# Performance work log

Hardware: AMD Instinct MI355X
Metric: run time of the kernel (lower is better)

Reference implementation:

```python
import jax, jax.numpy as jnp
import numpy as np

N_NODES = 50000
N_EDGES = 1600000
HID = 128
REST = 96  # (hidden//4) x 1e vectors = 32*3
N_MP = 2


def _linear_init(key, fan_in, fan_out):
    return jax.random.normal(key, (fan_in, fan_out), dtype=jnp.float32) / np.sqrt(fan_in)


def setup_inputs() -> dict:
    key = jax.random.key(0)
    ks = jax.random.split(key, 16)
    h = jax.random.normal(ks[0], (N_NODES, HID + REST), dtype=jnp.float32)
    edge_index = jax.random.randint(ks[1], (2, N_EDGES), 0, N_NODES, dtype=jnp.int32)
    edge_len = jax.random.uniform(ks[2], (N_EDGES,), dtype=jnp.float32) * 5.0
    # ScalarMessagePassing MLPs: Linear(2*HID+1 -> HID), SiLU, Linear(HID -> HID), stacked per layer
    mp_w1 = jnp.stack([_linear_init(ks[3 + i], 2 * HID + 1, HID) for i in range(N_MP)])
    mp_b1 = jnp.zeros((N_MP, HID), dtype=jnp.float32)
    mp_w2 = jnp.stack([_linear_init(ks[5 + i], HID, HID) for i in range(N_MP)])
    mp_b2 = jnp.zeros((N_MP, HID), dtype=jnp.float32)
    # NodeUpdateMLP: Linear(HID -> HID), SiLU, Linear(HID -> HID)
    nu_w1 = _linear_init(ks[7], HID, HID)
    nu_b1 = jnp.zeros((HID,), dtype=jnp.float32)
    nu_w2 = _linear_init(ks[8], HID, HID)
    nu_b2 = jnp.zeros((HID,), dtype=jnp.float32)
    return dict(h=h, edge_index=edge_index, edge_len=edge_len,
                mp_w1=mp_w1, mp_b1=mp_b1, mp_w2=mp_w2, mp_b2=mp_b2,
                nu_w1=nu_w1, nu_b1=nu_b1, nu_w2=nu_w2, nu_b2=nu_b2)


def _scalar_mp(scalars, sender, receiver, edge_len, w1, b1, w2, b2):
    # gather -> MLP -> index_add scatter, residual on scalar channels
    msg_in = jnp.concatenate([scalars[sender], scalars[receiver], edge_len[:, None]], axis=-1)  # [E, 2H+1]
    msgs = jax.nn.silu(msg_in @ w1 + b1) @ w2 + b2  # [E, H]
    agg = jax.ops.segment_sum(msgs, receiver, num_segments=scalars.shape[0])  # [N, H]
    return scalars + agg


def reference(h, edge_index, edge_len, mp_w1, mp_b1, mp_w2, mp_b2, nu_w1, nu_b1, nu_w2, nu_b2):
    scalars, rest = h[..., :HID], h[..., HID:]
    sender, receiver = edge_index[0], edge_index[1]
    for i in range(N_MP):
        scalars = _scalar_mp(scalars, sender, receiver, edge_len,
                             mp_w1[i], mp_b1[i], mp_w2[i], mp_b2[i])
    # NodeUpdateMLP: scalars + MLP(scalars)
    scalars = scalars + (jax.nn.silu(scalars @ nu_w1 + nu_b1) @ nu_w2 + nu_b2)
    return jnp.concatenate([scalars, rest], axis=-1)
```

## Files before the change

### kernel.cpp

```cpp
#include <hip/hip_runtime.h>
#include <hip/hip_fp16.h>


#define NFEAT 224
#define RBITS 8
#define NB 196
#define CAP 10240

typedef _Float16 v8h __attribute__((ext_vector_type(8)));
typedef _Float16 v2h __attribute__((ext_vector_type(2)));
typedef float f32x4 __attribute__((ext_vector_type(4)));

#define MFMA16(a, b, c) __builtin_amdgcn_mfma_f32_16x16x32_f16(a, b, c, 0, 0, 0)

__device__ __forceinline__ float silu_f(float x) {
    float e = __expf(-x);
    return x * __builtin_amdgcn_rcpf(1.0f + e);
}

__global__ void k_prep(const float* __restrict__ mp_w1, const float* __restrict__ mp_w2,
                       const float* __restrict__ nu_w1, const float* __restrict__ nu_w2,
                       _Float16* __restrict__ Wp, int* __restrict__ cnt,
                       const float4* __restrict__ h4, float4* __restrict__ out4, int N) {
    if (blockIdx.x < 8) {
        const float* srcs[8] = {
            mp_w1, mp_w1 + 16384, mp_w2,
            mp_w1 + 32896, mp_w1 + 32896 + 16384, mp_w2 + 16384,
            nu_w1, nu_w2
        };
        const float* W = srcs[blockIdx.x];
        _Float16* dst = Wp + (size_t)blockIdx.x * 16384;
        for (int i = 0; i < 8; ++i) {
            int u = threadIdx.x + i * 256;
            int nt = u >> 8;
            int kt = (u >> 6) & 3;
            int lane = u & 63;
            int kb = kt * 32 + (lane >> 4) * 8;
            int n = nt * 16 + (lane & 15);
#pragma unroll
            for (int j = 0; j < 8; ++j)
                dst[(size_t)u * 8 + j] = (_Float16)W[(size_t)(kb + j) * 128 + n];
        }
    } else {
        int b = blockIdx.x - 8;
        int t = threadIdx.x;
        if (b == 0 && t < NB) cnt[t] = 0;
        if (t < 240) {
            int r = b * 10 + t / 24;
            int c = t % 24;
            if (r < N) out4[(size_t)r * 56 + 32 + c] = h4[(size_t)r * 56 + 32 + c];
        }
    }
}

__global__ void cs_bucket(const int* __restrict__ recv, const int* __restrict__ sender,
                          const float* __restrict__ elen, int* __restrict__ cnt,
                          uint2* __restrict__ bp, int E, int chunk) {
    __shared__ int lhist[256];
    __shared__ int lcur[256];
    int t = threadIdx.x;
    int start = blockIdx.x * chunk;
    int end = start + chunk; if (end > E) end = E;
    lhist[t] = 0;
    __syncthreads();
    int rv[16];
#pragma unroll
    for (int j = 0; j < 16; ++j) {
        int i = start + t + j * 256;
        rv[j] = (i < end) ? recv[i] : -1;
        if (rv[j] >= 0) atomicAdd(&lhist[rv[j] >> RBITS], 1);
    }
    __syncthreads();
    if (t < NB) {
        int c = lhist[t];
        lcur[t] = t * CAP + (c ? atomicAdd(&cnt[t], c) : 0);
    }
    __syncthreads();
#pragma unroll
    for (int j = 0; j < 16; ++j) {
        int i = start + t + j * 256;
        if (i < end) {
            int r = rv[j];
            int pos = atomicAdd(&lcur[r >> RBITS], 1);
            unsigned pay = (unsigned)sender[i] |
                           ((unsigned)__half_as_ushort(__float2half_rn(elen[i])) << 16);
            bp[pos] = make_uint2((unsigned)r, pay);
        }
    }
}

__global__ void cs_csr(const int* __restrict__ cnt, const uint2* __restrict__ bp,
                       int* __restrict__ deg, int* __restrict__ rowstart,
                       unsigned* __restrict__ epack, int N) {
    __shared__ int hist[256];
    __shared__ int sh[256];
    __shared__ int lcur[256];
    int t = threadIdx.x;
    int b = blockIdx.x;
    int r0 = b << RBITS;
    int e0 = b * CAP;
    int e1 = e0 + cnt[b];
    hist[t] = 0;
    __syncthreads();
    for (int i = e0 + t; i < e1; i += 256)
        atomicAdd(&hist[(int)(bp[i].x & 255u)], 1);
    __syncthreads();
    sh[t] = hist[t];
    __syncthreads();
    for (int off = 1; off < 256; off <<= 1) {
        int add = (t >= off) ? sh[t - off] : 0;
        __syncthreads();
        sh[t] += add;
        __syncthreads();
    }
    int excl = (t == 0) ? 0 : sh[t - 1];
    lcur[t] = e0 + excl;
    int r = r0 + t;
    if (r < N) { deg[r] = hist[t]; rowstart[r] = e0 + excl; }
    __syncthreads();
    for (int i = e0 + t; i < e1; i += 256) {
        uint2 e = bp[i];
        int pos = atomicAdd(&lcur[(int)(e.x & 255u)], 1);
        epack[pos] = e.y;
    }
}


#define MM_STAGE_A_F32(Aptr, ldA)                                           \
    _Pragma("unroll") for (int i = 0; i < 4; ++i) {                         \
        int u = threadIdx.x + i * 256;                                      \
        int r = u >> 4;                                                     \
        int g = u & 15;                                                     \
        int gr = blockIdx.x * 64 + r;                                       \
        float4 x0 = make_float4(0.f, 0.f, 0.f, 0.f);                        \
        float4 x1 = x0;                                                     \
        if (gr < M) {                                                       \
            const float* s_ = (Aptr) + (size_t)gr * (ldA) + g * 8;          \
            x0 = *(const float4*)s_;                                        \
            x1 = *(const float4*)(s_ + 4);                                  \
        }                                                                   \
        v8h hv;                                                             \
        hv[0] = (_Float16)x0.x; hv[1] = (_Float16)x0.y;                     \
        hv[2] = (_Float16)x0.z; hv[3] = (_Float16)x0.w;                     \
        hv[4] = (_Float16)x1.x; hv[5] = (_Float16)x1.y;                     \
        hv[6] = (_Float16)x1.z; hv[7] = (_Float16)x1.w;                     \
        Af[((r >> 4) * 4 + (g >> 2)) * 64 + (g & 3) * 16 + (r & 15)] = hv;  \
    }

#define MM_STAGE_A_F16(Aptr)                                                \
    _Pragma("unroll") for (int i = 0; i < 4; ++i) {                         \
        int u = threadIdx.x + i * 256;                                      \
        int r = u >> 4;                                                     \
        int g = u & 15;                                                     \
        int gr = blockIdx.x * 64 + r;                                       \
        float4 x = make_float4(0.f, 0.f, 0.f, 0.f);                         \
        if (gr < M) x = *(const float4*)((Aptr) + (size_t)gr * 128 + g * 8);\
        *(float4*)&Af[((r >> 4) * 4 + (g >> 2)) * 64 + (g & 3) * 16 + (r & 15)] = x; \
    }

#define MM_WAVE_PROLOG                                                      \
    __syncthreads();                                                        \
    const int wv = threadIdx.x >> 6;                                        \
    const int lane = threadIdx.x & 63;                                      \
    const int q_ = lane >> 4;                                               \
    const int c0_ = lane & 15;                                              \
    v8h a0 = Af[(wv * 4 + 0) * 64 + lane];                                  \
    v8h a1 = Af[(wv * 4 + 1) * 64 + lane];                                  \
    v8h a2 = Af[(wv * 4 + 2) * 64 + lane];                                  \
    v8h a3 = Af[(wv * 4 + 3) * 64 + lane];                                  \
    const int grb = blockIdx.x * 64 + wv * 16 + q_ * 4;

#define MM_RELOAD_A(SRC)                                                    \
    a0 = SRC[(wv * 4 + 0) * 64 + lane];                                     \
    a1 = SRC[(wv * 4 + 1) * 64 + lane];                                     \
    a2 = SRC[(wv * 4 + 2) * 64 + lane];                                     \
    a3 = SRC[(wv * 4 + 3) * 64 + lane];

#define MM_COMPUTE_B(WPTR, ...)                                             \
    {                                                                       \
        const v8h* Bp_ = (const v8h*)(WPTR) + lane;                         \
        _Pragma("unroll") for (int nt = 0; nt < 8; ++nt) {                  \
            v8h b0 = Bp_[nt * 256];                                         \
            v8h b1v = Bp_[nt * 256 + 64];                                   \
            v8h b2v = Bp_[nt * 256 + 128];                                  \
            v8h b3v = Bp_[nt * 256 + 192];                                  \
            f32x4 c = {0.f, 0.f, 0.f, 0.f};                                 \
            c = MFMA16(a0, b0, c);                                          \
            c = MFMA16(a1, b1v, c);                                         \
            c = MFMA16(a2, b2v, c);                                         \
            c = MFMA16(a3, b3v, c);                                         \
            const int col = nt * 16 + c0_;                                  \
            __VA_ARGS__                                                     \
        }                                                                   \
    }

#define MM_EXCHANGE_IDX                                                     \
    int kt = col >> 5;                                                      \
    int o = col & 31;                                                       \
    int qp = o >> 3;                                                        \
    int j = o & 7;                                                          \
    int base = ((wv * 4 + kt) * 64 + qp * 16 + q_ * 4) * 8 + j;

__launch_bounds__(256)
__global__ void k_mm_xsrb2(const float* __restrict__ A, int ldA,
                           const _Float16* __restrict__ Wp0, const float* __restrict__ b1,
                           _Float16* __restrict__ Xs, _Float16* __restrict__ Xrb, int M) {
    __shared__ v8h Af[1024];
    MM_STAGE_A_F32(A, ldA)
    MM_WAVE_PROLOG
    MM_COMPUTE_B(Wp0, {
        _Pragma("unroll") for (int i = 0; i < 4; ++i) {
            int gr = grb + i;
            if (gr < M) Xs[(size_t)gr * 128 + col] = (_Float16)c[i];
        }
    })
    MM_COMPUTE_B(Wp0 + 16384, {
        float bc = b1[col];
        _Pragma("unroll") for (int i = 0; i < 4; ++i) {
            int gr = grb + i;
            if (gr < M) Xrb[(size_t)gr * 128 + col] = (_Float16)(c[i] + bc);
        }
    })
}

__launch_bounds__(256)
__global__ void k_mm_accxsrb(const _Float16* __restrict__ P, const _Float16* __restrict__ Ww2,
                             const float* __restrict__ b2, const int* __restrict__ deg,
                             const float* __restrict__ Sin, int ldSin,
                             float* __restrict__ Sout,
                             const _Float16* __restrict__ Wp1, const float* __restrict__ b1,
                             _Float16* __restrict__ Xs, _Float16* __restrict__ Xrb, int M) {
    __shared__ v8h Af[1024];
    __shared__ v8h Af2[1024];
    MM_STAGE_A_F16(P)
    MM_WAVE_PROLOG
    _Float16* A2 = (_Float16*)Af2;
    MM_COMPUTE_B(Ww2, {
        float bc = b2[col];
        MM_EXCHANGE_IDX
        _Pragma("unroll") for (int i = 0; i < 4; ++i) {
            int gr = grb + i;
            float sv = 0.f;
            if (gr < M) {
                sv = Sin[(size_t)gr * ldSin + col] + c[i] + bc * (float)deg[gr];
                Sout[(size_t)gr * 128 + col] = sv;
            }
            A2[base + i * 8] = (_Float16)sv;
        }
    })
    __syncthreads();
    MM_RELOAD_A(Af2)
    MM_COMPUTE_B(Wp1, {
        _Pragma("unroll") for (int i = 0; i < 4; ++i) {
            int gr = grb + i;
            if (gr < M) Xs[(size_t)gr * 128 + col] = (_Float16)c[i];
        }
    })
    MM_COMPUTE_B(Wp1 + 16384, {
        float bc = b1[col];
        _Pragma("unroll") for (int i = 0; i < 4; ++i) {
            int gr = grb + i;
            if (gr < M) Xrb[(size_t)gr * 128 + col] = (_Float16)(c[i] + bc);
        }
    })
}

__launch_bounds__(256)
__global__ void k_mm_accnode(const _Float16* __restrict__ P, const _Float16* __restrict__ Ww2,
                             const float* __restrict__ b2, const int* __restrict__ deg,
                             const float* __restrict__ Sin,
                             const _Float16* __restrict__ Wn1, const float* __restrict__ nb1,
                             const _Float16* __restrict__ Wn2, const float* __restrict__ nb2,
                             float* __restrict__ out, int M) {
    __shared__ v8h Af[1024];
    __shared__ v8h Af2[1024];
    MM_STAGE_A_F16(P)
    MM_WAVE_PROLOG
    float s2v[8][4];
    _Float16* A2 = (_Float16*)Af2;
    MM_COMPUTE_B(Ww2, {
        float bc = b2[col];
        MM_EXCHANGE_IDX
        _Pragma("unroll") for (int i = 0; i < 4; ++i) {
            int gr = grb + i;
            float sv = 0.f;
            if (gr < M) sv = Sin[(size_t)gr * 128 + col] + c[i] + bc * (float)deg[gr];
            s2v[nt][i] = sv;
            A2[base + i * 8] = (_Float16)sv;
        }
    })
    __syncthreads();
    MM_RELOAD_A(Af2)
    _Float16* A3 = (_Float16*)Af;
    MM_COMPUTE_B(Wn1, {
        float bc = nb1[col];
        MM_EXCHANGE_IDX
        _Pragma("unroll") for (int i = 0; i < 4; ++i)
            A3[base + i * 8] = (_Float16)silu_f(c[i] + bc);
    })
    __syncthreads();
    MM_RELOAD_A(Af)
    MM_COMPUTE_B(Wn2, {
        float bc = nb2[col];
        _Pragma("unroll") for (int i = 0; i < 4; ++i) {
            int gr = grb + i;
            if (gr < M)
                out[(size_t)gr * NFEAT + col] = s2v[nt][i] + c[i] + bc;
        }
    })
}

__device__ __forceinline__ v2h silu2_pk(v2h pre) {
    const v2h hp3 = {(_Float16)3.f, (_Float16)3.f};
    const v2h hn3 = {(_Float16)-3.f, (_Float16)-3.f};
    v2h h = pre * (_Float16)0.5f;
    v2h z = __builtin_elementwise_min(__builtin_elementwise_max(h, hn3), hp3);
    v2h w = z * z;
    v2h f = w * (_Float16)0.00033637f + (_Float16)-0.0074935f;
    f = f * w + (_Float16)0.063236f;
    f = f * w + (_Float16)-0.280292f;
    f = f * w + (_Float16)0.988137f;
    v2h u = z * f;
    return h * u + h;
}

__launch_bounds__(256)
__global__ void k_edge(const v2h* __restrict__ Xs, const v2h* __restrict__ Xrb,
                       const float* __restrict__ w1L, const unsigned* __restrict__ epack,
                       const int* __restrict__ rowstart, const int* __restrict__ deg,
                       v2h* __restrict__ P, int N) {
    int wid = (blockIdx.x * blockDim.x + threadIdx.x) >> 6;
    int lane = threadIdx.x & 63;
    if (wid >= N) return;
    int lo = __builtin_amdgcn_readfirstlane(rowstart[wid]);
    int dg = __builtin_amdgcn_readfirstlane(deg[wid]);
    const unsigned* ep = epack + lo;
    v2h xr = Xrb[(size_t)wid * 64 + lane];
    float2 wlf = *(const float2*)(w1L + lane * 2);
    v2h wl = {(_Float16)wlf.x, (_Float16)wlf.y};
    float ax = 0.f, ay = 0.f;
    int k = 0;
    unsigned pc[8];
    v2h xc[8];
    if (dg >= 8) {
#pragma unroll
        for (int u = 0; u < 8; ++u) pc[u] = ep[u];
#pragma unroll
        for (int u = 0; u < 8; ++u)
            xc[u] = Xs[(size_t)(pc[u] & 0xFFFFu) * 64 + lane];
    }
    for (; k + 16 <= dg; k += 8) {
        unsigned pn[8];
        v2h xn[8];
#pragma unroll
        for (int u = 0; u < 8; ++u) pn[u] = ep[k + 8 + u];
#pragma unroll
        for (int u = 0; u < 8; ++u)
            xn[u] = Xs[(size_t)(pn[u] & 0xFFFFu) * 64 + lane];
        v2h t2 = {(_Float16)0.f, (_Float16)0.f};
#pragma unroll
        for (int u = 0; u < 8; ++u) {
            _Float16 lv = __builtin_bit_cast(_Float16, (unsigned short)(pc[u] >> 16));
            v2h pre = xc[u] + xr + lv * wl;
            t2 = t2 + silu2_pk(pre);
        }
        ax += (float)t2[0]; ay += (float)t2[1];
#pragma unroll
        for (int u = 0; u < 8; ++u) { pc[u] = pn[u]; xc[u] = xn[u]; }
    }
    if (k + 8 <= dg) {
        v2h t2 = {(_Float16)0.f, (_Float16)0.f};
#pragma unroll
        for (int u = 0; u < 8; ++u) {
            _Float16 lv = __builtin_bit_cast(_Float16, (unsigned short)(pc[u] >> 16));
            v2h pre = xc[u] + xr + lv * wl;
            t2 = t2 + silu2_pk(pre);
        }
        ax += (float)t2[0]; ay += (float)t2[1];
        k += 8;
    }
    for (; k < dg; ++k) {
        unsigned p = ep[k];
        _Float16 lv = __builtin_bit_cast(_Float16, (unsigned short)(p >> 16));
        v2h x = Xs[(size_t)(p & 0xFFFFu) * 64 + lane];
        v2h pre = x + xr + lv * wl;
        v2h s = silu2_pk(pre);
        ax += (float)s[0]; ay += (float)s[1];
    }
    v2h o = {(_Float16)ax, (_Float16)ay};
    P[(size_t)wid * 64 + lane] = o;
}

extern "C" void kernel_launch(void* const* d_in, const int* in_sizes, int n_in,
                              void* d_out, int out_size, void* d_ws, size_t ws_size,
                              hipStream_t stream) {
    const float* h      = (const float*)d_in[0];
    const int*   eidx   = (const int*)d_in[1];
    const float* elen   = (const float*)d_in[2];
    const float* mp_w1  = (const float*)d_in[3];
    const float* mp_b1  = (const float*)d_in[4];
    const float* mp_w2  = (const float*)d_in[5];
    const float* mp_b2  = (const float*)d_in[6];
    const float* nu_w1  = (const float*)d_in[7];
    const float* nu_b1  = (const float*)d_in[8];
    const float* nu_w2  = (const float*)d_in[9];
    const float* nu_b2  = (const float*)d_in[10];
    float* out = (float*)d_out;

    const int N = in_sizes[0] / NFEAT;
    const int E = in_sizes[2];
    const int* sender   = eidx;
    const int* receiver = eidx + E;

    char* w = (char*)d_ws;
    auto alloc = [&](size_t bytes) -> char* {
        char* p = w;
        w += (bytes + 255) & ~(size_t)255;
        return p;
    };
    float*    S1    = (float*)alloc((size_t)N * 128 * 4);
    _Float16* Pf    = (_Float16*)alloc((size_t)N * 128 * 2);
    _Float16* Xs16  = (_Float16*)alloc((size_t)N * 128 * 2);
    _Float16* Xrb16 = (_Float16*)alloc((size_t)N * 128 * 2);
    _Float16* Wp    = (_Float16*)alloc((size_t)8 * 16384 * 2);
    uint2*    bp    = (uint2*)alloc((size_t)NB * CAP * 8);
    unsigned* epack = (unsigned*)alloc((size_t)NB * CAP * 4);
    int*      deg      = (int*)alloc((size_t)N * 4);
    int*      rowstart = (int*)alloc((size_t)N * 4);
    int*      cnt      = (int*)alloc((size_t)NB * 4);

    k_prep<<<8 + (N + 9) / 10, 256, 0, stream>>>(mp_w1, mp_w2, nu_w1, nu_w2, Wp, cnt,
                                                 (const float4*)h, (float4*)out, N);
    const int chunk = 4096;
    cs_bucket<<<(E + chunk - 1) / chunk, 256, 0, stream>>>(receiver, sender, elen, cnt,
                                                           bp, E, chunk);
    cs_csr<<<NB, 256, 0, stream>>>(cnt, bp, deg, rowstart, epack, N);

    const int gb = (N + 63) / 64;
    const int eb = (N * 64 + 255) / 256;

    k_mm_xsrb2<<<gb, 256, 0, stream>>>(h, NFEAT, Wp, mp_b1, Xs16, Xrb16, N);
    k_edge<<<eb, 256, 0, stream>>>((const v2h*)Xs16, (const v2h*)Xrb16,
                                   mp_w1 + 32768, epack, rowstart, deg, (v2h*)Pf, N);
    k_mm_accxsrb<<<gb, 256, 0, stream>>>(Pf, Wp + (size_t)2 * 16384, mp_b2, deg,
                                         h, NFEAT, S1,
                                         Wp + (size_t)3 * 16384, mp_b1 + 128,
                                         Xs16, Xrb16, N);
    k_edge<<<eb, 256, 0, stream>>>((const v2h*)Xs16, (const v2h*)Xrb16,
                                   mp_w1 + 32896 + 32768, epack, rowstart, deg,
                                   (v2h*)Pf, N);
    k_mm_accnode<<<gb, 256, 0, stream>>>(Pf, Wp + (size_t)5 * 16384, mp_b2 + 128, deg,
                                         S1,
                                         Wp + (size_t)6 * 16384, nu_b1,
                                         Wp + (size_t)7 * 16384, nu_b2,
                                         out, N);
}
```

Measured before the change: 356.5 us.

## Fuse preprocessing kernels and fold silu half-scale into node projections

Merges weight packing with edge bucketing, and merges CSR build, the first node projection GEMM and the rest-channel copy into one launch with block-range dispatch. The counter zeroing moves to a memset. The 0.5 pre-scale used by the tanh-based silu is folded into the Xs/Xrb outputs and the edge-length weight, which removes a multiply per edge element. The aim is to cut launch count and serialization between independent stages, at the cost of mixing heterogeneous block roles within one grid.

```diff
diff --git a/kernel.cpp b/kernel.cpp
--- a/kernel.cpp
+++ b/kernel.cpp
@@ -6,6 +6,7 @@
 #define RBITS 8
 #define NB 196
 #define CAP 10240
+#define COPYB 512
 
 typedef _Float16 v8h __attribute__((ext_vector_type(8)));
 typedef _Float16 v2h __attribute__((ext_vector_type(2)));
@@ -18,10 +19,14 @@
     return x * __builtin_amdgcn_rcpf(1.0f + e);
 }
 
-__global__ void k_prep(const float* __restrict__ mp_w1, const float* __restrict__ mp_w2,
-                       const float* __restrict__ nu_w1, const float* __restrict__ nu_w2,
-                       _Float16* __restrict__ Wp, int* __restrict__ cnt,
-                       const float4* __restrict__ h4, float4* __restrict__ out4, int N) {
+__global__ void k_packbucket(const float* __restrict__ mp_w1, const float* __restrict__ mp_w2,
+                             const float* __restrict__ nu_w1, const float* __restrict__ nu_w2,
+                             _Float16* __restrict__ Wp,
+                             const int* __restrict__ recv, const int* __restrict__ sender,
+                             const float* __restrict__ elen, int* __restrict__ cnt,
+                             uint2* __restrict__ bp, int E) {
+    __shared__ int lhist[256];
+    __shared__ int lcur[256];
     if (blockIdx.x < 8) {
         const float* srcs[8] = {
             mp_w1, mp_w1 + 16384, mp_w2,
@@ -41,26 +46,11 @@
             for (int j = 0; j < 8; ++j)
                 dst[(size_t)u * 8 + j] = (_Float16)W[(size_t)(kb + j) * 128 + n];
         }
-    } else {
-        int b = blockIdx.x - 8;
-        int t = threadIdx.x;
-        if (b == 0 && t < NB) cnt[t] = 0;
-        if (t < 240) {
-            int r = b * 10 + t / 24;
-            int c = t % 24;
-            if (r < N) out4[(size_t)r * 56 + 32 + c] = h4[(size_t)r * 56 + 32 + c];
-        }
-    }
-}
-
-__global__ void cs_bucket(const int* __restrict__ recv, const int* __restrict__ sender,
-                          const float* __restrict__ elen, int* __restrict__ cnt,
-                          uint2* __restrict__ bp, int E, int chunk) {
-    __shared__ int lhist[256];
-    __shared__ int lcur[256];
+        return;
+    }
     int t = threadIdx.x;
-    int start = blockIdx.x * chunk;
-    int end = start + chunk; if (end > E) end = E;
+    int start = (blockIdx.x - 8) * 4096;
+    int end = start + 4096; if (end > E) end = E;
     lhist[t] = 0;
     __syncthreads();
     int rv[16];
@@ -89,49 +79,13 @@
     }
 }
 
-__global__ void cs_csr(const int* __restrict__ cnt, const uint2* __restrict__ bp,
-                       int* __restrict__ deg, int* __restrict__ rowstart,
-                       unsigned* __restrict__ epack, int N) {
-    __shared__ int hist[256];
-    __shared__ int sh[256];
-    __shared__ int lcur[256];
-    int t = threadIdx.x;
-    int b = blockIdx.x;
-    int r0 = b << RBITS;
-    int e0 = b * CAP;
-    int e1 = e0 + cnt[b];
-    hist[t] = 0;
-    __syncthreads();
-    for (int i = e0 + t; i < e1; i += 256)
-        atomicAdd(&hist[(int)(bp[i].x & 255u)], 1);
-    __syncthreads();
-    sh[t] = hist[t];
-    __syncthreads();
-    for (int off = 1; off < 256; off <<= 1) {
-        int add = (t >= off) ? sh[t - off] : 0;
-        __syncthreads();
-        sh[t] += add;
-        __syncthreads();
-    }
-    int excl = (t == 0) ? 0 : sh[t - 1];
-    lcur[t] = e0 + excl;
-    int r = r0 + t;
-    if (r < N) { deg[r] = hist[t]; rowstart[r] = e0 + excl; }
-    __syncthreads();
-    for (int i = e0 + t; i < e1; i += 256) {
-        uint2 e = bp[i];
-        int pos = atomicAdd(&lcur[(int)(e.x & 255u)], 1);
-        epack[pos] = e.y;
-    }
-}
-
 
 #define MM_STAGE_A_F32(Aptr, ldA)                                           \
     _Pragma("unroll") for (int i = 0; i < 4; ++i) {                         \
         int u = threadIdx.x + i * 256;                                      \
         int r = u >> 4;                                                     \
         int g = u & 15;                                                     \
-        int gr = blockIdx.x * 64 + r;                                       \
+        int gr = mm_bx * 64 + r;                                            \
         float4 x0 = make_float4(0.f, 0.f, 0.f, 0.f);                        \
         float4 x1 = x0;                                                     \
         if (gr < M) {                                                       \
@@ -152,7 +106,7 @@
         int u = threadIdx.x + i * 256;                                      \
         int r = u >> 4;                                                     \
         int g = u & 15;                                                     \
-        int gr = blockIdx.x * 64 + r;                                       \
+        int gr = mm_bx * 64 + r;                                            \
         float4 x = make_float4(0.f, 0.f, 0.f, 0.f);                         \
         if (gr < M) x = *(const float4*)((Aptr) + (size_t)gr * 128 + g * 8);\
         *(float4*)&Af[((r >> 4) * 4 + (g >> 2)) * 64 + (g & 3) * 16 + (r & 15)] = x; \
@@ -168,7 +122,7 @@
     v8h a1 = Af[(wv * 4 + 1) * 64 + lane];                                  \
     v8h a2 = Af[(wv * 4 + 2) * 64 + lane];                                  \
     v8h a3 = Af[(wv * 4 + 3) * 64 + lane];                                  \
-    const int grb = blockIdx.x * 64 + wv * 16 + q_ * 4;
+    const int grb = mm_bx * 64 + wv * 16 + q_ * 4;
 
 #define MM_RELOAD_A(SRC)                                                    \
     a0 = SRC[(wv * 4 + 0) * 64 + lane];                                     \
@@ -202,25 +156,74 @@
     int base = ((wv * 4 + kt) * 64 + qp * 16 + q_ * 4) * 8 + j;
 
 __launch_bounds__(256)
-__global__ void k_mm_xsrb2(const float* __restrict__ A, int ldA,
-                           const _Float16* __restrict__ Wp0, const float* __restrict__ b1,
-                           _Float16* __restrict__ Xs, _Float16* __restrict__ Xrb, int M) {
-    __shared__ v8h Af[1024];
-    MM_STAGE_A_F32(A, ldA)
-    MM_WAVE_PROLOG
-    MM_COMPUTE_B(Wp0, {
-        _Pragma("unroll") for (int i = 0; i < 4; ++i) {
-            int gr = grb + i;
-            if (gr < M) Xs[(size_t)gr * 128 + col] = (_Float16)c[i];
-        }
-    })
-    MM_COMPUTE_B(Wp0 + 16384, {
-        float bc = b1[col];
-        _Pragma("unroll") for (int i = 0; i < 4; ++i) {
-            int gr = grb + i;
-            if (gr < M) Xrb[(size_t)gr * 128 + col] = (_Float16)(c[i] + bc);
-        }
-    })
+__global__ void k_csr_xsrb_copy(const int* __restrict__ cnt, const uint2* __restrict__ bp,
+                                int* __restrict__ deg, int* __restrict__ rowstart,
+                                unsigned* __restrict__ epack,
+                                const float* __restrict__ A,
+                                const _Float16* __restrict__ Wp0, const float* __restrict__ b1,
+                                _Float16* __restrict__ Xs, _Float16* __restrict__ Xrb, int M,
+                                const float4* __restrict__ h4, float4* __restrict__ out4) {
+    __shared__ v8h AfB[1024];
+    const int gb = (M + 63) >> 6;
+    if (blockIdx.x < NB) {
+        int* hist = (int*)AfB;
+        int* sh = hist + 256;
+        int* lcur = sh + 256;
+        int t = threadIdx.x;
+        int b = blockIdx.x;
+        int r0 = b << RBITS;
+        int e0 = b * CAP;
+        int e1 = e0 + cnt[b];
+        hist[t] = 0;
+        __syncthreads();
+        for (int i = e0 + t; i < e1; i += 256)
+            atomicAdd(&hist[(int)(bp[i].x & 255u)], 1);
+        __syncthreads();
+        sh[t] = hist[t];
+        __syncthreads();
+        for (int off = 1; off < 256; off <<= 1) {
+            int add = (t >= off) ? sh[t - off] : 0;
+            __syncthreads();
+            sh[t] += add;
+            __syncthreads();
+        }
+        int excl = (t == 0) ? 0 : sh[t - 1];
+        lcur[t] = e0 + excl;
+        int r = r0 + t;
+        if (r < M) { deg[r] = hist[t]; rowstart[r] = e0 + excl; }
+        __syncthreads();
+        for (int i = e0 + t; i < e1; i += 256) {
+            uint2 e = bp[i];
+            int pos = atomicAdd(&lcur[(int)(e.x & 255u)], 1);
+            epack[pos] = e.y;
+        }
+    } else if (blockIdx.x < NB + gb) {
+        v8h* const Af = AfB;
+        const int mm_bx = blockIdx.x - NB;
+        MM_STAGE_A_F32(A, NFEAT)
+        MM_WAVE_PROLOG
+        MM_COMPUTE_B(Wp0, {
+            _Pragma("unroll") for (int i = 0; i < 4; ++i) {
+                int gr = grb + i;
+                if (gr < M) Xs[(size_t)gr * 128 + col] = (_Float16)(c[i] * 0.5f);
+            }
+        })
+        MM_COMPUTE_B(Wp0 + 16384, {
+            float bc = b1[col];
+            _Pragma("unroll") for (int i = 0; i < 4; ++i) {
+                int gr = grb + i;
+                if (gr < M) Xrb[(size_t)gr * 128 + col] = (_Float16)((c[i] + bc) * 0.5f);
+            }
+        })
+    } else {
+        int bid = blockIdx.x - NB - gb;
+        int total = M * 24;
+        for (int idx = bid * 256 + threadIdx.x; idx < total; idx += COPYB * 256) {
+            int r = idx / 24;
+            int c = idx - r * 24;
+            out4[(size_t)r * 56 + 32 + c] = h4[(size_t)r * 56 + 32 + c];
+        }
+    }
 }
 
 __launch_bounds__(256)
@@ -232,6 +235,7 @@
                              _Float16* __restrict__ Xs, _Float16* __restrict__ Xrb, int M) {
     __shared__ v8h Af[1024];
     __shared__ v8h Af2[1024];
+    const int mm_bx = blockIdx.x;
     MM_STAGE_A_F16(P)
     MM_WAVE_PROLOG
     _Float16* A2 = (_Float16*)Af2;
@@ -253,14 +257,14 @@
     MM_COMPUTE_B(Wp1, {
         _Pragma("unroll") for (int i = 0; i < 4; ++i) {
             int gr = grb + i;
-            if (gr < M) Xs[(size_t)gr * 128 + col] = (_Float16)c[i];
+            if (gr < M) Xs[(size_t)gr * 128 + col] = (_Float16)(c[i] * 0.5f);
         }
     })
     MM_COMPUTE_B(Wp1 + 16384, {
         float bc = b1[col];
         _Pragma("unroll") for (int i = 0; i < 4; ++i) {
             int gr = grb + i;
-            if (gr < M) Xrb[(size_t)gr * 128 + col] = (_Float16)(c[i] + bc);
+            if (gr < M) Xrb[(size_t)gr * 128 + col] = (_Float16)((c[i] + bc) * 0.5f);
         }
     })
 }
@@ -274,6 +278,7 @@
                              float* __restrict__ out, int M) {
     __shared__ v8h Af[1024];
     __shared__ v8h Af2[1024];
+    const int mm_bx = blockIdx.x;
     MM_STAGE_A_F16(P)
     MM_WAVE_PROLOG
     float s2v[8][4];
@@ -310,10 +315,9 @@
     })
 }
 
-__device__ __forceinline__ v2h silu2_pk(v2h pre) {
+__device__ __forceinline__ v2h silu2_pk_h(v2h h) {
     const v2h hp3 = {(_Float16)3.f, (_Float16)3.f};
     const v2h hn3 = {(_Float16)-3.f, (_Float16)-3.f};
-    v2h h = pre * (_Float16)0.5f;
     v2h z = __builtin_elementwise_min(__builtin_elementwise_max(h, hn3), hp3);
     v2h w = z * z;
     v2h f = w * (_Float16)0.00033637f + (_Float16)-0.0074935f;
@@ -337,7 +341,7 @@
     const unsigned* ep = epack + lo;
     v2h xr = Xrb[(size_t)wid * 64 + lane];
     float2 wlf = *(const float2*)(w1L + lane * 2);
-    v2h wl = {(_Float16)wlf.x, (_Float16)wlf.y};
+    v2h wl = {(_Float16)(wlf.x * 0.5f), (_Float16)(wlf.y * 0.5f)};
     float ax = 0.f, ay = 0.f;
     int k = 0;
     unsigned pc[8];
@@ -361,8 +365,8 @@
 #pragma unroll
         for (int u = 0; u < 8; ++u) {
             _Float16 lv = __builtin_bit_cast(_Float16, (unsigned short)(pc[u] >> 16));
-            v2h pre = xc[u] + xr + lv * wl;
-            t2 = t2 + silu2_pk(pre);
+            v2h h = xc[u] + xr + lv * wl;
+            t2 = t2 + silu2_pk_h(h);
         }
         ax += (float)t2[0]; ay += (float)t2[1];
 #pragma unroll
@@ -373,8 +377,8 @@
 #pragma unroll
         for (int u = 0; u < 8; ++u) {
             _Float16 lv = __builtin_bit_cast(_Float16, (unsigned short)(pc[u] >> 16));
-            v2h pre = xc[u] + xr + lv * wl;
-            t2 = t2 + silu2_pk(pre);
+            v2h h = xc[u] + xr + lv * wl;
+            t2 = t2 + silu2_pk_h(h);
         }
         ax += (float)t2[0]; ay += (float)t2[1];
         k += 8;
@@ -383,8 +387,8 @@
         unsigned p = ep[k];
         _Float16 lv = __builtin_bit_cast(_Float16, (unsigned short)(p >> 16));
         v2h x = Xs[(size_t)(p & 0xFFFFu) * 64 + lane];
-        v2h pre = x + xr + lv * wl;
-        v2h s = silu2_pk(pre);
+        v2h h = x + xr + lv * wl;
+        v2h s = silu2_pk_h(h);
         ax += (float)s[0]; ay += (float)s[1];
     }
     v2h o = {(_Float16)ax, (_Float16)ay};
@@ -429,17 +433,18 @@
     int*      rowstart = (int*)alloc((size_t)N * 4);
     int*      cnt      = (int*)alloc((size_t)NB * 4);
 
-    k_prep<<<8 + (N + 9) / 10, 256, 0, stream>>>(mp_w1, mp_w2, nu_w1, nu_w2, Wp, cnt,
-                                                 (const float4*)h, (float4*)out, N);
-    const int chunk = 4096;
-    cs_bucket<<<(E + chunk - 1) / chunk, 256, 0, stream>>>(receiver, sender, elen, cnt,
-                                                           bp, E, chunk);
-    cs_csr<<<NB, 256, 0, stream>>>(cnt, bp, deg, rowstart, epack, N);
+    (void)hipMemsetAsync(cnt, 0, (size_t)NB * 4, stream);
 
     const int gb = (N + 63) / 64;
     const int eb = (N * 64 + 255) / 256;
-
-    k_mm_xsrb2<<<gb, 256, 0, stream>>>(h, NFEAT, Wp, mp_b1, Xs16, Xrb16, N);
+    const int bb = (E + 4095) / 4096;
+
+    k_packbucket<<<8 + bb, 256, 0, stream>>>(mp_w1, mp_w2, nu_w1, nu_w2, Wp,
+                                             receiver, sender, elen, cnt, bp, E);
+    k_csr_xsrb_copy<<<NB + gb + COPYB, 256, 0, stream>>>(cnt, bp, deg, rowstart, epack,
+                                                         h, Wp, mp_b1,
+                                                         Xs16, Xrb16, N,
+                                                         (const float4*)h, (float4*)out);
     k_edge<<<eb, 256, 0, stream>>>((const v2h*)Xs16, (const v2h*)Xrb16,
                                    mp_w1 + 32768, epack, rowstart, deg, (v2h*)Pf, N);
     k_mm_accxsrb<<<gb, 256, 0, stream>>>(Pf, Wp + (size_t)2 * 16384, mp_b2, deg,
```

Result: faster. 338.7 us (-5.0%).
